# Optimization experiments

Hardware: AMD Instinct MI355X
Metric: run time of the kernel (lower is better)

## Reference

```python
import jax, jax.numpy as jnp
import numpy as np

B, C_IN, N, T, E, C_OUT = 128, 32, 325, 24, 3, 64


def setup_inputs() -> dict:
    key = jax.random.key(0)
    kx, ka, kw, kb = jax.random.split(key, 4)
    x = jax.random.normal(kx, (B, C_IN, N, T), dtype=jnp.float32)
    supports = jax.random.normal(ka, (E, N, N), dtype=jnp.float32) * (1.0 / np.sqrt(N))
    # 1x1 Conv2d params: weight [c_out, c_in*(edge_dim+1)], bias [c_out]
    fan_in = C_IN * (E + 1)
    W = jax.random.normal(kw, (C_OUT, fan_in), dtype=jnp.float32) * (1.0 / np.sqrt(fan_in))
    b = jax.random.normal(kb, (C_OUT,), dtype=jnp.float32) * 0.05
    return {"x": x, "supports": supports, "W": W, "b": b}


def reference(x, supports, W, b):
    # x: [B, C, N, T], supports: [E, N, N]
    Bb, C, Nn, Tt = x.shape
    # nconv for every support at once: einsum 'bcvt,vw->bcwt' batched over E
    diff = jnp.einsum('bcvt,evw->becwt', x, supports)  # [B, E, C, N, T]
    # concat [x] + diffused copies along channel dim -> [B, (E+1)*C, N, T]
    h = jnp.concatenate([x[:, None], diff], axis=1).reshape(Bb, -1, Nn, Tt)
    # 1x1 conv == channel-mixing matmul; squeeze(-1) is a no-op since T > 1
    out = jnp.einsum('bkvt,ok->bovt', h, W) + b[None, :, None, None]
    return out  # [B, c_out, N, T]
```

## Files before the change

### kernel.cpp

```cpp
#include <hip/hip_runtime.h>
#include <hip/hip_bf16.h>

typedef short bf16x8 __attribute__((ext_vector_type(8)));
typedef short bf16x4 __attribute__((ext_vector_type(4)));
typedef float f32x4  __attribute__((ext_vector_type(4)));

static constexpr int Bb   = 128;
static constexpr int Cin  = 32;
static constexpr int Nn   = 325;
static constexpr int Tt   = 24;
static constexpr int Cout = 64;
static constexpr int NKS  = 11;
static constexpr int WP   = 336;
static constexpr int NWT  = 21;
static constexpr int OS1  = 210;
static constexpr size_t XTB_ELEMS = (size_t)Bb * NKS * (Tt * Cin) * 32;
static constexpr size_t STP_ELEMS = (size_t)4 * NKS * WP * 32;
static constexpr size_t WB_ELEMS  = (size_t)Cout * 128;

__device__ __forceinline__ void gld16(const void* g, void* l) {
    __builtin_amdgcn_global_load_lds(
        (const __attribute__((address_space(1))) void*)g,
        (__attribute__((address_space(3))) void*)l, 16, 0, 0);
}
__device__ __forceinline__ short bfb(float f) {
    __hip_bfloat16 h = __float2bfloat16(f);
    return *reinterpret_cast<short*>(&h);
}

__global__ void build_stp(const float* __restrict__ sup,
                          __hip_bfloat16* __restrict__ stpb) {
    int idx = blockIdx.x * 256 + threadIdx.x;
    int total = 4 * NKS * WP * 32;
    if (idx >= total) return;
    int e  = idx / (NKS * WP * 32);
    int r  = idx % (NKS * WP * 32);
    int ks = r / (WP * 32);
    int r2 = r % (WP * 32);
    int w  = r2 / 32;
    int vi = r2 % 32;
    int v  = ks * 32 + vi;
    float val = 0.f;
    if (e == 0) {
        val = (v == w && v < Nn) ? 1.f : 0.f;
    } else if (v < Nn && w < Nn) {
        val = sup[((size_t)(e - 1) * Nn + v) * Nn + w];
    }
    stpb[idx] = __float2bfloat16(val);
}

__global__ void build_wb(const float* __restrict__ W,
                         __hip_bfloat16* __restrict__ Wb) {
    int i = blockIdx.x * 256 + threadIdx.x;
    if (i < Cout * 128) Wb[i] = __float2bfloat16(W[i]);
}

__global__ void transpose_x(const float* __restrict__ x,
                            __hip_bfloat16* __restrict__ xTb) {
    __shared__ __hip_bfloat16 ls[Cin * 32 * 28];
    int xcd = blockIdx.x & 7;
    int idx = blockIdx.x >> 3;
    int b   = xcd * 16 + idx / NKS;
    int ks  = idx % NKS;
    int tid = threadIdx.x;
    for (int i = 0; i < 24; ++i) {
        int f4 = i * 256 + tid;
        int c  = f4 / 192;
        int rm = f4 % 192;
        int vi = rm / 6;
        int t0 = (rm % 6) * 4;
        int v  = ks * 32 + vi;
        float4 val = make_float4(0.f, 0.f, 0.f, 0.f);
        if (v < Nn)
            val = *(const float4*)(x + (((size_t)(b * Cin + c) * Nn + v) * Tt + t0));
        bf16x4 pk = { bfb(val.x), bfb(val.y), bfb(val.z), bfb(val.w) };
        *(bf16x4*)&ls[(c * 32 + vi) * 28 + t0] = pk;
    }
    __syncthreads();
    for (int j = 0; j < 12; ++j) {
        int o    = j * 256 + tid;
        int row  = o >> 2;
        int slot = o & 3;
        int t = row >> 5, c = row & 31;
        union { short us[8]; bf16x8 v8; } pk;
#pragma unroll
        for (int q = 0; q < 8; ++q) {
            __hip_bfloat16 h = ls[(c * 32 + slot * 8 + q) * 28 + t];
            pk.us[q] = *reinterpret_cast<short*>(&h);
        }
        *(bf16x8*)((char*)xTb + ((size_t)(b * NKS + ks) * 768 + row) * 64 + slot * 16) = pk.v8;
    }
}

__global__ __launch_bounds__(256, 2) void graphconv_main(
    const __hip_bfloat16* __restrict__ xTb,
    const __hip_bfloat16* __restrict__ stpb,
    const __hip_bfloat16* __restrict__ Wb,
    const float* __restrict__ bias,
    float* __restrict__ out) {
    __shared__ alignas(16) __hip_bfloat16 Ss[44 * 512];
    __shared__ float Os[16 * OS1];

    int bid = blockIdx.x;
    int lg  = (bid & 7) * 672 + (bid >> 3);
    int b   = lg / 42;
    int r   = lg % 42;
    int wt  = r >> 1, th = r & 1;
    int w0  = wt * 16;

    int tid = threadIdx.x, wid = tid >> 6, lane = tid & 63;
    int cl = lane & 15, kg = lane >> 4;

    const char* xslab = (const char*)xTb + (size_t)b * NKS * 768 * 64;
    const char* xbase = xslab + (size_t)(th * 384 + wid * 96 + cl) * 64 + kg * 16;

    {
        int srow  = lane >> 2;
        int sslot = ((lane & 3) ^ ((lane >> 3) & 3)) << 4;
        for (int i = wid; i < 44; i += 4) {
            int e = i / NKS, ks = i % NKS;
            gld16((const char*)stpb +
                      ((size_t)((e * NKS + ks) * WP) + w0 + srow) * 64 + sslot,
                  (char*)&Ss[0] + i * 1024 + lane * 16);
        }
    }

    bf16x8 xf[3][6];
#pragma unroll
    for (int s = 0; s < 2; ++s)
#pragma unroll
        for (int j = 0; j < 6; ++j)
            xf[s][j] = *(const bf16x8*)(xbase + (size_t)s * 49152 + (size_t)j * 1024);

    __syncthreads();

    const int asw = (kg ^ ((cl >> 1) & 3)) << 4;
    bf16x8 af[2][4];
#pragma unroll
    for (int e = 0; e < 4; ++e)
        af[0][e] = *(const bf16x8*)((const char*)&Ss[0] +
                                    (size_t)(e * NKS) * 1024 + cl * 64 + asw);

    f32x4 acc1[4][6] = {};
#pragma unroll
    for (int ks = 0; ks < NKS; ++ks) {
        const int cur3 = ks % 3, pf3 = (ks + 2) % 3;
        const int cur2 = ks & 1, nx2 = cur2 ^ 1;
        if (ks + 2 < NKS) {
#pragma unroll
            for (int j = 0; j < 6; ++j)
                xf[pf3][j] = *(const bf16x8*)(xbase + (size_t)(ks + 2) * 49152 +
                                              (size_t)j * 1024);
        }
        if (ks + 1 < NKS) {
#pragma unroll
            for (int e = 0; e < 4; ++e)
                af[nx2][e] = *(const bf16x8*)((const char*)&Ss[0] +
                                 (size_t)(e * NKS + ks + 1) * 1024 + cl * 64 + asw);
        }
        __builtin_amdgcn_s_setprio(1);
#pragma unroll
        for (int e = 0; e < 4; ++e)
#pragma unroll
            for (int j = 0; j < 6; ++j)
                acc1[e][j] = __builtin_amdgcn_mfma_f32_16x16x32_bf16(
                    xf[cur3][j], af[cur2][e], acc1[e][j], 0, 0, 0);
        __builtin_amdgcn_s_setprio(0);
    }

    f32x4 acc2[4][3] = {};
#pragma unroll
    for (int kappa = 0; kappa < 8; ++kappa) {
        const int e = kappa >> 1, half = kappa & 1;
        bf16x4 wf[4];
#pragma unroll
        for (int mt = 0; mt < 4; ++mt)
            wf[mt] = *(const bf16x4*)((const char*)Wb + (mt * 16 + cl) * 256 +
                                      kappa * 32 + kg * 8);
#pragma unroll
        for (int tj = 0; tj < 3; ++tj) {
            const int j = tj * 2 + half;
            f32x4 y = acc1[e][j];
            bf16x4 pb = { bfb(y[0]), bfb(y[1]), bfb(y[2]), bfb(y[3]) };
#pragma unroll
            for (int mt = 0; mt < 4; ++mt)
                acc2[mt][tj] = __builtin_amdgcn_mfma_f32_16x16x16bf16_1k(
                    wf[mt], pb, acc2[mt][tj], 0, 0, 0);
        }
    }

#pragma unroll
    for (int p = 0; p < 4; ++p) {
        if (p) __syncthreads();
#pragma unroll
        for (int tj = 0; tj < 3; ++tj) {
            const int t = wid * 3 + tj;
#pragma unroll
            for (int r2_ = 0; r2_ < 4; ++r2_)
                Os[(kg * 4 + r2_) * OS1 + cl * 13 + t] = acc2[p][tj][r2_];
        }
        __syncthreads();
        const int o2 = tid >> 4, w = tid & 15;
        const int wg = w0 + w;
        if (wg < Nn) {
            const int o = p * 16 + o2;
            const float bv = bias[o];
            float f[12];
#pragma unroll
            for (int q = 0; q < 12; ++q)
                f[q] = Os[o2 * OS1 + w * 13 + q] + bv;
            float* op = out + ((size_t)(b * Cout + o) * Nn + wg) * Tt + th * 12;
#pragma unroll
            for (int q = 0; q < 3; ++q)
                *(float4*)(op + q * 4) =
                    make_float4(f[q * 4], f[q * 4 + 1], f[q * 4 + 2], f[q * 4 + 3]);
        }
    }
}

extern "C" void kernel_launch(void* const* d_in, const int* in_sizes, int n_in,
                              void* d_out, int out_size, void* d_ws, size_t ws_size,
                              hipStream_t stream) {
    const float* x    = (const float*)d_in[0];
    const float* sup  = (const float*)d_in[1];
    const float* W    = (const float*)d_in[2];
    const float* bias = (const float*)d_in[3];
    float* out = (float*)d_out;

    __hip_bfloat16* xTb  = (__hip_bfloat16*)d_ws;
    __hip_bfloat16* stpb = xTb + XTB_ELEMS;
    __hip_bfloat16* Wb   = stpb + STP_ELEMS;

    build_stp<<<(int)((STP_ELEMS + 255) / 256), 256, 0, stream>>>(sup, stpb);
    build_wb<<<(int)((WB_ELEMS + 255) / 256), 256, 0, stream>>>(W, Wb);
    transpose_x<<<Bb * NKS, 256, 0, stream>>>(x, xTb);
    graphconv_main<<<Bb * NWT * 2, 256, 0, stream>>>(xTb, stpb, Wb, bias, out);
}
```

Baseline: 309.0 us.

## Drop identity support matmul, retile main kernel to 32-wide node tiles with 512 threads

Removes the explicit identity matrix from the stacked supports, so the x-passthrough is no longer a full 11-step matmul. A single MFMA step against an in-register one-hot fragment, run only on the matching k-slab, extracts it instead. The main kernel is retiled to 32 output nodes by 8 time steps per block, with 512 threads, thirds of the time axis, and a shared LDS buffer reused for the output staging. This cuts about a quarter of the first-stage MFMA work and changes occupancy and reuse, at the cost of a more intricate epilogue and a one-hot trick that must line up exactly with the x tile layout.

Measured after the change: 507.7 us. 64.3% more time.

```diff
diff --git a/kernel.cpp b/kernel.cpp
--- a/kernel.cpp
+++ b/kernel.cpp
@@ -11,11 +11,11 @@
 static constexpr int Tt   = 24;
 static constexpr int Cout = 64;
 static constexpr int NKS  = 11;
-static constexpr int WP   = 336;
-static constexpr int NWT  = 21;
-static constexpr int OS1  = 210;
+static constexpr int WP2  = 352;
+static constexpr int NWTB = 11;
+static constexpr int NTH  = 3;
 static constexpr size_t XTB_ELEMS = (size_t)Bb * NKS * (Tt * Cin) * 32;
-static constexpr size_t STP_ELEMS = (size_t)4 * NKS * WP * 32;
+static constexpr size_t STP_ELEMS = (size_t)3 * NKS * WP2 * 32;
 static constexpr size_t WB_ELEMS  = (size_t)Cout * 128;
 
 __device__ __forceinline__ void gld16(const void* g, void* l) {
@@ -31,21 +31,18 @@
 __global__ void build_stp(const float* __restrict__ sup,
                           __hip_bfloat16* __restrict__ stpb) {
     int idx = blockIdx.x * 256 + threadIdx.x;
-    int total = 4 * NKS * WP * 32;
+    int total = 3 * NKS * WP2 * 32;
     if (idx >= total) return;
-    int e  = idx / (NKS * WP * 32);
-    int r  = idx % (NKS * WP * 32);
-    int ks = r / (WP * 32);
-    int r2 = r % (WP * 32);
+    int ep = idx / (NKS * WP2 * 32);
+    int r  = idx % (NKS * WP2 * 32);
+    int ks = r / (WP2 * 32);
+    int r2 = r % (WP2 * 32);
     int w  = r2 / 32;
     int vi = r2 % 32;
     int v  = ks * 32 + vi;
     float val = 0.f;
-    if (e == 0) {
-        val = (v == w && v < Nn) ? 1.f : 0.f;
-    } else if (v < Nn && w < Nn) {
-        val = sup[((size_t)(e - 1) * Nn + v) * Nn + w];
-    }
+    if (v < Nn && w < Nn)
+        val = sup[((size_t)ep * Nn + v) * Nn + w];
     stpb[idx] = __float2bfloat16(val);
 }
 
@@ -92,128 +89,162 @@
     }
 }
 
-__global__ __launch_bounds__(256, 2) void graphconv_main(
+__global__ __launch_bounds__(512, 4) void graphconv_main(
     const __hip_bfloat16* __restrict__ xTb,
     const __hip_bfloat16* __restrict__ stpb,
     const __hip_bfloat16* __restrict__ Wb,
     const float* __restrict__ bias,
     float* __restrict__ out) {
-    __shared__ alignas(16) __hip_bfloat16 Ss[44 * 512];
-    __shared__ float Os[16 * OS1];
+    __shared__ alignas(16) char smem[33 * 2048];
+    __hip_bfloat16* Ss = (__hip_bfloat16*)smem;
+    float*          Os = (float*)smem;
 
     int bid = blockIdx.x;
-    int lg  = (bid & 7) * 672 + (bid >> 3);
-    int b   = lg / 42;
-    int r   = lg % 42;
-    int wt  = r >> 1, th = r & 1;
-    int w0  = wt * 16;
+    int lg  = (bid & 7) * 528 + (bid >> 3);
+    int b   = lg / 33;
+    int r   = lg % 33;
+    int wt  = r / NTH;
+    int th  = r % NTH;
+    int w0  = wt * 32, t0 = th * 8, ct0 = th * 256;
 
     int tid = threadIdx.x, wid = tid >> 6, lane = tid & 63;
     int cl = lane & 15, kg = lane >> 4;
 
-    const char* xslab = (const char*)xTb + (size_t)b * NKS * 768 * 64;
-    const char* xbase = xslab + (size_t)(th * 384 + wid * 96 + cl) * 64 + kg * 16;
+    const char* xbase = (const char*)xTb + (size_t)b * NKS * 768 * 64 +
+                        (size_t)(ct0 + wid * 32 + cl) * 64 + kg * 16;
 
     {
         int srow  = lane >> 2;
         int sslot = ((lane & 3) ^ ((lane >> 3) & 3)) << 4;
-        for (int i = wid; i < 44; i += 4) {
-            int e = i / NKS, ks = i % NKS;
-            gld16((const char*)stpb +
-                      ((size_t)((e * NKS + ks) * WP) + w0 + srow) * 64 + sslot,
-                  (char*)&Ss[0] + i * 1024 + lane * 16);
-        }
-    }
-
-    bf16x8 xf[3][6];
+        for (int q = wid; q < 66; q += 8) {
+            int slab = q >> 1, half = q & 1;
+            gld16((const char*)stpb + (size_t)slab * 22528 +
+                      (size_t)(w0 + half * 16 + srow) * 64 + sslot,
+                  (char*)smem + slab * 2048 + half * 1024 + lane * 16);
+        }
+    }
+
+    bf16x8 xf[3][2];
 #pragma unroll
     for (int s = 0; s < 2; ++s)
 #pragma unroll
-        for (int j = 0; j < 6; ++j)
-            xf[s][j] = *(const bf16x8*)(xbase + (size_t)s * 49152 + (size_t)j * 1024);
+        for (int j = 0; j < 2; ++j)
+            xf[s][j] = *(const bf16x8*)(xbase + (size_t)s * 49152 + j * 1024);
+
+    bf16x8 af0[2];
+#pragma unroll
+    for (int wf = 0; wf < 2; ++wf) {
+        short hot = (kg == wf * 2 + (cl >> 3)) ? (short)0x3F80 : (short)0;
+        int he = cl & 7;
+        bf16x8 z = { 0, 0, 0, 0, 0, 0, 0, 0 };
+#pragma unroll
+        for (int i = 0; i < 8; ++i)
+            if (he == i) z[i] = hot;
+        af0[wf] = z;
+    }
 
     __syncthreads();
 
     const int asw = (kg ^ ((cl >> 1) & 3)) << 4;
-    bf16x8 af[2][4];
-#pragma unroll
-    for (int e = 0; e < 4; ++e)
-        af[0][e] = *(const bf16x8*)((const char*)&Ss[0] +
-                                    (size_t)(e * NKS) * 1024 + cl * 64 + asw);
-
-    f32x4 acc1[4][6] = {};
+    bf16x8 af[2][3][2];
+#pragma unroll
+    for (int ep = 0; ep < 3; ++ep)
+#pragma unroll
+        for (int wf = 0; wf < 2; ++wf)
+            af[0][ep][wf] = *(const bf16x8*)((const char*)Ss +
+                (size_t)(ep * NKS) * 2048 + (wf * 16 + cl) * 64 + asw);
+
+    f32x4 acc1[3][2][2] = {};
+    f32x4 aid[2][2]     = {};
 #pragma unroll
     for (int ks = 0; ks < NKS; ++ks) {
         const int cur3 = ks % 3, pf3 = (ks + 2) % 3;
         const int cur2 = ks & 1, nx2 = cur2 ^ 1;
         if (ks + 2 < NKS) {
 #pragma unroll
-            for (int j = 0; j < 6; ++j)
-                xf[pf3][j] = *(const bf16x8*)(xbase + (size_t)(ks + 2) * 49152 +
-                                              (size_t)j * 1024);
+            for (int j = 0; j < 2; ++j)
+                xf[pf3][j] = *(const bf16x8*)(xbase + (size_t)(ks + 2) * 49152 + j * 1024);
         }
         if (ks + 1 < NKS) {
 #pragma unroll
-            for (int e = 0; e < 4; ++e)
-                af[nx2][e] = *(const bf16x8*)((const char*)&Ss[0] +
-                                 (size_t)(e * NKS + ks + 1) * 1024 + cl * 64 + asw);
+            for (int ep = 0; ep < 3; ++ep)
+#pragma unroll
+                for (int wf = 0; wf < 2; ++wf)
+                    af[nx2][ep][wf] = *(const bf16x8*)((const char*)Ss +
+                        (size_t)(ep * NKS + ks + 1) * 2048 + (wf * 16 + cl) * 64 + asw);
         }
         __builtin_amdgcn_s_setprio(1);
 #pragma unroll
-        for (int e = 0; e < 4; ++e)
-#pragma unroll
-            for (int j = 0; j < 6; ++j)
-                acc1[e][j] = __builtin_amdgcn_mfma_f32_16x16x32_bf16(
-                    xf[cur3][j], af[cur2][e], acc1[e][j], 0, 0, 0);
+        for (int ep = 0; ep < 3; ++ep)
+#pragma unroll
+            for (int wf = 0; wf < 2; ++wf)
+#pragma unroll
+                for (int j = 0; j < 2; ++j)
+                    acc1[ep][wf][j] = __builtin_amdgcn_mfma_f32_16x16x32_bf16(
+                        xf[cur3][j], af[cur2][ep][wf], acc1[ep][wf][j], 0, 0, 0);
+        if (ks == wt) {
+#pragma unroll
+            for (int wf = 0; wf < 2; ++wf)
+#pragma unroll
+                for (int j = 0; j < 2; ++j)
+                    aid[wf][j] = __builtin_amdgcn_mfma_f32_16x16x32_bf16(
+                        xf[cur3][j], af0[wf], aid[wf][j], 0, 0, 0);
+        }
         __builtin_amdgcn_s_setprio(0);
     }
 
-    f32x4 acc2[4][3] = {};
+    f32x4 acc2[4][2] = {};
 #pragma unroll
     for (int kappa = 0; kappa < 8; ++kappa) {
-        const int e = kappa >> 1, half = kappa & 1;
-        bf16x4 wf[4];
+        const int es = kappa >> 1, h = kappa & 1;
+        bf16x4 wfr[4];
 #pragma unroll
         for (int mt = 0; mt < 4; ++mt)
-            wf[mt] = *(const bf16x4*)((const char*)Wb + (mt * 16 + cl) * 256 +
-                                      kappa * 32 + kg * 8);
-#pragma unroll
-        for (int tj = 0; tj < 3; ++tj) {
-            const int j = tj * 2 + half;
-            f32x4 y = acc1[e][j];
+            wfr[mt] = *(const bf16x4*)((const char*)Wb + (mt * 16 + cl) * 256 +
+                                       kappa * 32 + kg * 8);
+#pragma unroll
+        for (int wf = 0; wf < 2; ++wf) {
+            f32x4 y = (es == 0) ? aid[wf][h] : acc1[es - 1][wf][h];
             bf16x4 pb = { bfb(y[0]), bfb(y[1]), bfb(y[2]), bfb(y[3]) };
 #pragma unroll
             for (int mt = 0; mt < 4; ++mt)
-                acc2[mt][tj] = __builtin_amdgcn_mfma_f32_16x16x16bf16_1k(
-                    wf[mt], pb, acc2[mt][tj], 0, 0, 0);
-        }
-    }
-
-#pragma unroll
-    for (int p = 0; p < 4; ++p) {
+                acc2[mt][wf] = __builtin_amdgcn_mfma_f32_16x16x16bf16_1k(
+                    wfr[mt], pb, acc2[mt][wf], 0, 0, 0);
+        }
+    }
+
+    __syncthreads();
+#pragma unroll
+    for (int p = 0; p < 2; ++p) {
         if (p) __syncthreads();
 #pragma unroll
-        for (int tj = 0; tj < 3; ++tj) {
-            const int t = wid * 3 + tj;
-#pragma unroll
-            for (int r2_ = 0; r2_ < 4; ++r2_)
-                Os[(kg * 4 + r2_) * OS1 + cl * 13 + t] = acc2[p][tj][r2_];
+        for (int mh = 0; mh < 2; ++mh) {
+            const int mt = p * 2 + mh;
+#pragma unroll
+            for (int wf = 0; wf < 2; ++wf)
+#pragma unroll
+                for (int r2_ = 0; r2_ < 4; ++r2_) {
+                    int ol = mh * 16 + kg * 4 + r2_;
+                    Os[(ol * 32 + wf * 16 + cl) * 9 + wid] = acc2[mt][wf][r2_];
+                }
         }
         __syncthreads();
-        const int o2 = tid >> 4, w = tid & 15;
-        const int wg = w0 + w;
-        if (wg < Nn) {
-            const int o = p * 16 + o2;
-            const float bv = bias[o];
-            float f[12];
-#pragma unroll
-            for (int q = 0; q < 12; ++q)
-                f[q] = Os[o2 * OS1 + w * 13 + q] + bv;
-            float* op = out + ((size_t)(b * Cout + o) * Nn + wg) * Tt + th * 12;
-#pragma unroll
-            for (int q = 0; q < 3; ++q)
-                *(float4*)(op + q * 4) =
-                    make_float4(f[q * 4], f[q * 4 + 1], f[q * 4 + 2], f[q * 4 + 3]);
+#pragma unroll
+        for (int hh = 0; hh < 2; ++hh) {
+            int pair = hh * 512 + tid;
+            int ol = pair >> 5, w = pair & 31;
+            int o  = p * 32 + ol;
+            int wg = w0 + w;
+            if (wg < Nn) {
+                float bv = bias[o];
+                float f[8];
+#pragma unroll
+                for (int q = 0; q < 8; ++q)
+                    f[q] = Os[(ol * 32 + w) * 9 + q] + bv;
+                float* op = out + ((size_t)(b * Cout + o) * Nn + wg) * Tt + t0;
+                *(float4*)op       = make_float4(f[0], f[1], f[2], f[3]);
+                *(float4*)(op + 4) = make_float4(f[4], f[5], f[6], f[7]);
+            }
         }
     }
 }
@@ -234,5 +265,5 @@
     build_stp<<<(int)((STP_ELEMS + 255) / 256), 256, 0, stream>>>(sup, stpb);
     build_wb<<<(int)((WB_ELEMS + 255) / 256), 256, 0, stream>>>(W, Wb);
     transpose_x<<<Bb * NKS, 256, 0, stream>>>(x, xTb);
-    graphconv_main<<<Bb * NWT * 2, 256, 0, stream>>>(xTb, stpb, Wb, bias, out);
-}
+    graphconv_main<<<Bb * NWTB * NTH, 512, 0, stream>>>(xTb, stpb, Wb, bias, out);
+}
```

## Stage x tiles through LDS with async loads, drop identity support, widen blocks

Applied to the files above, without the earlier changes.

The main kernel now runs 768 threads, one wave per time step, instead of 256. x tiles are streamed into a double-buffered LDS slab with global_load_lds and explicit vmcnt waits, replacing per-thread register prefetch. The identity support is no longer materialized as a dense matrix. Its contribution is computed by one extra MFMA against a one-hot fragment at a single k-step, which cuts the support MFMA and load work by a quarter. The change raises register and LDS pressure and adds fragile hand-written wait counts.

New measurement: 437.9 us. 41.7% more time.

```diff
diff --git a/kernel.cpp b/kernel.cpp
--- a/kernel.cpp
+++ b/kernel.cpp
@@ -11,11 +11,10 @@
 static constexpr int Tt   = 24;
 static constexpr int Cout = 64;
 static constexpr int NKS  = 11;
-static constexpr int WP   = 336;
+static constexpr int WP2  = 352;
 static constexpr int NWT  = 21;
-static constexpr int OS1  = 210;
 static constexpr size_t XTB_ELEMS = (size_t)Bb * NKS * (Tt * Cin) * 32;
-static constexpr size_t STP_ELEMS = (size_t)4 * NKS * WP * 32;
+static constexpr size_t STP_ELEMS = (size_t)3 * NKS * WP2 * 32;
 static constexpr size_t WB_ELEMS  = (size_t)Cout * 128;
 
 __device__ __forceinline__ void gld16(const void* g, void* l) {
@@ -31,21 +30,18 @@
 __global__ void build_stp(const float* __restrict__ sup,
                           __hip_bfloat16* __restrict__ stpb) {
     int idx = blockIdx.x * 256 + threadIdx.x;
-    int total = 4 * NKS * WP * 32;
+    int total = 3 * NKS * WP2 * 32;
     if (idx >= total) return;
-    int e  = idx / (NKS * WP * 32);
-    int r  = idx % (NKS * WP * 32);
-    int ks = r / (WP * 32);
-    int r2 = r % (WP * 32);
+    int ep = idx / (NKS * WP2 * 32);
+    int r  = idx % (NKS * WP2 * 32);
+    int ks = r / (WP2 * 32);
+    int r2 = r % (WP2 * 32);
     int w  = r2 / 32;
     int vi = r2 % 32;
     int v  = ks * 32 + vi;
     float val = 0.f;
-    if (e == 0) {
-        val = (v == w && v < Nn) ? 1.f : 0.f;
-    } else if (v < Nn && w < Nn) {
-        val = sup[((size_t)(e - 1) * Nn + v) * Nn + w];
-    }
+    if (v < Nn && w < Nn)
+        val = sup[((size_t)ep * Nn + v) * Nn + w];
     stpb[idx] = __float2bfloat16(val);
 }
 
@@ -92,128 +88,143 @@
     }
 }
 
-__global__ __launch_bounds__(256, 2) void graphconv_main(
+__global__ __launch_bounds__(768, 3) void graphconv_main(
     const __hip_bfloat16* __restrict__ xTb,
     const __hip_bfloat16* __restrict__ stpb,
     const __hip_bfloat16* __restrict__ Wb,
     const float* __restrict__ bias,
     float* __restrict__ out) {
-    __shared__ alignas(16) __hip_bfloat16 Ss[44 * 512];
-    __shared__ float Os[16 * OS1];
+    __shared__ alignas(16) char smem[2 * 24576 + 33 * 1024];
+    char* Ss = smem + 2 * 24576;
+    float* Os = (float*)smem;
 
     int bid = blockIdx.x;
     int lg  = (bid & 7) * 672 + (bid >> 3);
     int b   = lg / 42;
     int r   = lg % 42;
     int wt  = r >> 1, th = r & 1;
-    int w0  = wt * 16;
+    int w0  = wt * 16, t0 = th * 12;
 
     int tid = threadIdx.x, wid = tid >> 6, lane = tid & 63;
     int cl = lane & 15, kg = lane >> 4;
 
+    int srow  = lane >> 2;
+    int sslot = ((lane & 3) ^ ((lane >> 3) & 3)) << 4;
+    const int asw = (kg ^ ((cl >> 1) & 3)) << 4;
+
     const char* xslab = (const char*)xTb + (size_t)b * NKS * 768 * 64;
-    const char* xbase = xslab + (size_t)(th * 384 + wid * 96 + cl) * 64 + kg * 16;
-
+    const char* xsrc = xslab + (size_t)((t0 + wid) * 32 + srow) * 64 + sslot;
+    char* xdst = smem + wid * 2048 + lane * 16;
+
+    if (wid < 11) {
+#pragma unroll
+        for (int q = 0; q < 3; ++q) {
+            int i = wid * 3 + q;
+            gld16(stpb == nullptr ? nullptr :
+                  (const char*)stpb + ((size_t)i * WP2 + w0 + srow) * 64 + sslot,
+                  Ss + i * 1024 + lane * 16);
+        }
+    }
+#pragma unroll
+    for (int s = 0; s < 2; ++s)
+#pragma unroll
+        for (int q = 0; q < 2; ++q)
+            gld16(xsrc + (size_t)s * 49152 + q * 1024,
+                  xdst + s * 24576 + q * 1024);
+
+    bf16x8 idf;
     {
-        int srow  = lane >> 2;
-        int sslot = ((lane & 3) ^ ((lane >> 3) & 3)) << 4;
-        for (int i = wid; i < 44; i += 4) {
-            int e = i / NKS, ks = i % NKS;
-            gld16((const char*)stpb +
-                      ((size_t)((e * NKS + ks) * WP) + w0 + srow) * 64 + sslot,
-                  (char*)&Ss[0] + i * 1024 + lane * 16);
-        }
-    }
-
-    bf16x8 xf[3][6];
-#pragma unroll
-    for (int s = 0; s < 2; ++s)
-#pragma unroll
-        for (int j = 0; j < 6; ++j)
-            xf[s][j] = *(const bf16x8*)(xbase + (size_t)s * 49152 + (size_t)j * 1024);
-
-    __syncthreads();
-
-    const int asw = (kg ^ ((cl >> 1) & 3)) << 4;
-    bf16x8 af[2][4];
-#pragma unroll
-    for (int e = 0; e < 4; ++e)
-        af[0][e] = *(const bf16x8*)((const char*)&Ss[0] +
-                                    (size_t)(e * NKS) * 1024 + cl * 64 + asw);
-
-    f32x4 acc1[4][6] = {};
+        short hot = (kg == 2 * (wt & 1) + (cl >> 3)) ? (short)0x3F80 : (short)0;
+        bf16x8 z = { 0, 0, 0, 0, 0, 0, 0, 0 };
+#pragma unroll
+        for (int i = 0; i < 8; ++i)
+            z[i] = (i == (cl & 7)) ? hot : (short)0;
+        idf = z;
+    }
+
+    asm volatile("s_waitcnt vmcnt(4)" ::: "memory");
+    __syncthreads();
+    __builtin_amdgcn_sched_barrier(0);
+
+    f32x4 acc1[3][2] = {};
+    f32x4 aid[2]     = {};
+    const int id_ks = wt >> 1;
 #pragma unroll
     for (int ks = 0; ks < NKS; ++ks) {
-        const int cur3 = ks % 3, pf3 = (ks + 2) % 3;
-        const int cur2 = ks & 1, nx2 = cur2 ^ 1;
+        if (ks < 10) { asm volatile("s_waitcnt vmcnt(2)" ::: "memory"); }
+        else         { asm volatile("s_waitcnt vmcnt(0)" ::: "memory"); }
+        __builtin_amdgcn_sched_barrier(0);
+        const int bsel = (ks & 1) * 24576;
+        bf16x8 xf[2], af[3];
+#pragma unroll
+        for (int j = 0; j < 2; ++j)
+            xf[j] = *(const bf16x8*)(smem + bsel + wid * 2048 + j * 1024 +
+                                     cl * 64 + asw);
+#pragma unroll
+        for (int ep = 0; ep < 3; ++ep)
+            af[ep] = *(const bf16x8*)(Ss + (ep * NKS + ks) * 1024 + cl * 64 + asw);
+        __builtin_amdgcn_s_setprio(1);
+#pragma unroll
+        for (int ep = 0; ep < 3; ++ep)
+#pragma unroll
+            for (int j = 0; j < 2; ++j)
+                acc1[ep][j] = __builtin_amdgcn_mfma_f32_16x16x32_bf16(
+                    xf[j], af[ep], acc1[ep][j], 0, 0, 0);
+        if (ks == id_ks) {
+#pragma unroll
+            for (int j = 0; j < 2; ++j)
+                aid[j] = __builtin_amdgcn_mfma_f32_16x16x32_bf16(
+                    xf[j], idf, aid[j], 0, 0, 0);
+        }
+        __builtin_amdgcn_s_setprio(0);
         if (ks + 2 < NKS) {
-#pragma unroll
-            for (int j = 0; j < 6; ++j)
-                xf[pf3][j] = *(const bf16x8*)(xbase + (size_t)(ks + 2) * 49152 +
-                                              (size_t)j * 1024);
-        }
-        if (ks + 1 < NKS) {
-#pragma unroll
-            for (int e = 0; e < 4; ++e)
-                af[nx2][e] = *(const bf16x8*)((const char*)&Ss[0] +
-                                 (size_t)(e * NKS + ks + 1) * 1024 + cl * 64 + asw);
-        }
-        __builtin_amdgcn_s_setprio(1);
-#pragma unroll
-        for (int e = 0; e < 4; ++e)
-#pragma unroll
-            for (int j = 0; j < 6; ++j)
-                acc1[e][j] = __builtin_amdgcn_mfma_f32_16x16x32_bf16(
-                    xf[cur3][j], af[cur2][e], acc1[e][j], 0, 0, 0);
-        __builtin_amdgcn_s_setprio(0);
-    }
-
-    f32x4 acc2[4][3] = {};
+            asm volatile("s_waitcnt lgkmcnt(0)" ::: "memory");
+            __builtin_amdgcn_sched_barrier(0);
+#pragma unroll
+            for (int q = 0; q < 2; ++q)
+                gld16(xsrc + (size_t)(ks + 2) * 49152 + q * 1024,
+                      xdst + bsel + q * 1024);
+        }
+    }
+
+    f32x4 acc2[4] = {};
 #pragma unroll
     for (int kappa = 0; kappa < 8; ++kappa) {
-        const int e = kappa >> 1, half = kappa & 1;
-        bf16x4 wf[4];
-#pragma unroll
-        for (int mt = 0; mt < 4; ++mt)
-            wf[mt] = *(const bf16x4*)((const char*)Wb + (mt * 16 + cl) * 256 +
-                                      kappa * 32 + kg * 8);
-#pragma unroll
-        for (int tj = 0; tj < 3; ++tj) {
-            const int j = tj * 2 + half;
-            f32x4 y = acc1[e][j];
-            bf16x4 pb = { bfb(y[0]), bfb(y[1]), bfb(y[2]), bfb(y[3]) };
-#pragma unroll
-            for (int mt = 0; mt < 4; ++mt)
-                acc2[mt][tj] = __builtin_amdgcn_mfma_f32_16x16x16bf16_1k(
-                    wf[mt], pb, acc2[mt][tj], 0, 0, 0);
-        }
-    }
-
-#pragma unroll
-    for (int p = 0; p < 4; ++p) {
-        if (p) __syncthreads();
-#pragma unroll
-        for (int tj = 0; tj < 3; ++tj) {
-            const int t = wid * 3 + tj;
-#pragma unroll
-            for (int r2_ = 0; r2_ < 4; ++r2_)
-                Os[(kg * 4 + r2_) * OS1 + cl * 13 + t] = acc2[p][tj][r2_];
-        }
-        __syncthreads();
-        const int o2 = tid >> 4, w = tid & 15;
-        const int wg = w0 + w;
+        const int es = kappa >> 1, j = kappa & 1;
+        f32x4 y = (es == 0) ? aid[j] : acc1[es - 1][j];
+        bf16x4 pb = { bfb(y[0]), bfb(y[1]), bfb(y[2]), bfb(y[3]) };
+#pragma unroll
+        for (int mt = 0; mt < 4; ++mt) {
+            bf16x4 wf = *(const bf16x4*)((const char*)Wb + (mt * 16 + cl) * 256 +
+                                         kappa * 32 + kg * 8);
+            acc2[mt] = __builtin_amdgcn_mfma_f32_16x16x16bf16_1k(
+                wf, pb, acc2[mt], 0, 0, 0);
+        }
+    }
+
+    __syncthreads();
+#pragma unroll
+    for (int mt = 0; mt < 4; ++mt)
+#pragma unroll
+        for (int r2_ = 0; r2_ < 4; ++r2_) {
+            int o = mt * 16 + kg * 4 + r2_;
+            Os[o * 209 + cl * 13 + wid] = acc2[mt][r2_];
+        }
+    __syncthreads();
+    for (int pair = tid; pair < 1024; pair += 768) {
+        int o = pair >> 4, w = pair & 15;
+        int wg = w0 + w;
         if (wg < Nn) {
-            const int o = p * 16 + o2;
-            const float bv = bias[o];
+            float bv = bias[o];
             float f[12];
 #pragma unroll
             for (int q = 0; q < 12; ++q)
-                f[q] = Os[o2 * OS1 + w * 13 + q] + bv;
+                f[q] = Os[o * 209 + w * 13 + q] + bv;
             float* op = out + ((size_t)(b * Cout + o) * Nn + wg) * Tt + th * 12;
 #pragma unroll
-            for (int q = 0; q < 3; ++q)
-                *(float4*)(op + q * 4) =
-                    make_float4(f[q * 4], f[q * 4 + 1], f[q * 4 + 2], f[q * 4 + 3]);
+            for (int q3 = 0; q3 < 3; ++q3)
+                *(float4*)(op + q3 * 4) = make_float4(
+                    f[q3 * 4], f[q3 * 4 + 1], f[q3 * 4 + 2], f[q3 * 4 + 3]);
         }
     }
 }
@@ -234,5 +245,5 @@
     build_stp<<<(int)((STP_ELEMS + 255) / 256), 256, 0, stream>>>(sup, stpb);
     build_wb<<<(int)((WB_ELEMS + 255) / 256), 256, 0, stream>>>(W, Wb);
     transpose_x<<<Bb * NKS, 256, 0, stream>>>(x, xTb);
-    graphconv_main<<<Bb * NWT * 2, 256, 0, stream>>>(xTb, stpb, Wb, bias, out);
-}
+    graphconv_main<<<Bb * NWT * 2, 768, 0, stream>>>(xTb, stpb, Wb, bias, out);
+}
```
